# Kernel tuning notes

Hardware: AMD Instinct MI355X
Metric: run time of the kernel (lower is better)

The kernel has to match this reference:

```python
import jax, jax.numpy as jnp
import numpy as np

N = 100000      # nodes
E = 3200000     # directed edges
G = 1024        # graphs in batch


def setup_inputs() -> dict:
    key = jax.random.key(0)
    ks = jax.random.split(key, 12)
    x = jax.random.normal(ks[0], (N, 4), dtype=jnp.float32)
    edge_index = jax.random.randint(ks[1], (2, E), 0, N, dtype=jnp.int64)
    batch = jnp.sort(jax.random.randint(ks[2], (N,), 0, G, dtype=jnp.int64))
    s = 0.1
    return {
        'x': x, 'edge_index': edge_index, 'batch': batch,
        'W_emb': jax.random.normal(ks[3], (4, 1), jnp.float32) * s,
        'b_emb': jax.random.normal(ks[4], (4,), jnp.float32) * s,
        'W1': jax.random.normal(ks[5], (16, 7), jnp.float32) * s,
        'b1': jax.random.normal(ks[6], (16,), jnp.float32) * s,
        'W2': jax.random.normal(ks[7], (8, 16), jnp.float32) * s,
        'b2': jax.random.normal(ks[8], (8,), jnp.float32) * s,
        'W3': jax.random.normal(ks[9], (1, 8), jnp.float32) * s,
        'b3': jax.random.normal(ks[10], (1,), jnp.float32) * s,
    }


def _gcn_norm(edge_index, n):
    # add self-loops (PyG GCNConv default)
    loops = jnp.arange(n, dtype=edge_index.dtype)
    row = jnp.concatenate([edge_index[0], loops])  # source
    col = jnp.concatenate([edge_index[1], loops])  # target
    deg = jax.ops.segment_sum(jnp.ones_like(col, dtype=jnp.float32), col, num_segments=n)
    dinv = jnp.where(deg > 0, deg ** -0.5, 0.0)
    norm = dinv[row] * dinv[col]
    return row, col, norm


def _gcn_conv(h, W, b, row, col, norm, n):
    h = h @ W.T                                   # [n, out]
    msg = h[row] * norm[:, None]                  # gather + scale
    out = jax.ops.segment_sum(msg, col, num_segments=n)
    return out + b


def reference(x, edge_index, batch, W_emb, b_emb, W1, b1, W2, b2, W3, b3):
    row, col, norm = _gcn_norm(edge_index, N)
    atoms_vector = x[:, :1]
    atoms_xyz = x[:, 1:]
    one_hot_emb = atoms_vector @ W_emb.T + b_emb          # [N, 4]
    h = jnp.concatenate([one_hot_emb, atoms_xyz], axis=1) # [N, 7]
    h = jnp.tanh(_gcn_conv(h, W1, b1, row, col, norm, N)) # [N, 16]
    # dropout is identity in eval mode
    h = jnp.tanh(_gcn_conv(h, W2, b2, row, col, norm, N)) # [N, 8]
    # scatter-mean readout over graphs
    sums = jax.ops.segment_sum(h, batch, num_segments=G)
    cnts = jax.ops.segment_sum(jnp.ones((h.shape[0],), h.dtype), batch, num_segments=G)
    pooled = sums / jnp.maximum(cnts, 1.0)[:, None]       # [G, 8]
    return pooled @ W3.T + b3                             # [G, 1]
```

## Files before the change

kernel.cpp:

```cpp
#include <hip/hip_runtime.h>
#include <hip/hip_fp16.h>


constexpr int BLK  = 256;
constexpr int NPB  = 256;
constexpr int NBMX = 512;
constexpr int CAPB = 9216;
constexpr int PBLK = 512;
constexpr int CAPS = 6144;
constexpr int EPT  = 12;
constexpr int SBLK = 512;
constexpr int NIT4 = 5;
constexpr float S8 = 64.0f;

__global__ void k_place(const int4* __restrict__ row4, const int4* __restrict__ col4,
                        int* __restrict__ bucketCnt, unsigned int* __restrict__ data,
                        int E, int NB) {
    __shared__ unsigned int stage[CAPS];
    __shared__ int pos[NBMX], sstart[NBMX], lbase[NBMX];
    __shared__ int wsum[8];
    int t = threadIdx.x;
    int lane = t & 63, w = t >> 6;
    int begin = blockIdx.x * CAPS;
    int end = min(E, begin + CAPS);
    int csize = end - begin;
    int q0 = begin >> 2, q1 = end >> 2;
    if (t < NBMX) pos[t] = 0;
    __syncthreads();
    unsigned int ent[EPT];
    int meta[EPT];
#pragma unroll
    for (int it = 0; it < EPT / 4; it++) {
        int i = q0 + t + it * PBLK;
        bool ok = i < q1;
        int4 c = ok ? col4[i] : make_int4(0, 0, 0, 0);
        int4 r = ok ? row4[i] : make_int4(0, 0, 0, 0);
#pragma unroll
        for (int k = 0; k < 4; k++) {
            int cc = ((const int*)&c)[k];
            int rr = ((const int*)&r)[k];
            int b = cc >> 8;
            int o = ok ? atomicAdd(&pos[b], 1) : 0;
            ent[it * 4 + k] = ((unsigned int)(cc & 255) << 17) | (unsigned int)rr;
            meta[it * 4 + k] = ok ? ((b << 13) | o) : -1;
        }
    }
    __syncthreads();
    int v = pos[t];
    int sc = v;
#pragma unroll
    for (int off = 1; off < 64; off <<= 1) {
        int o = __shfl_up(sc, off, 64);
        if (lane >= off) sc += o;
    }
    if (lane == 63) wsum[w] = sc;
    __syncthreads();
    int pre = 0;
#pragma unroll
    for (int i = 0; i < 8; i++) if (i < w) pre += wsum[i];
    int excl = sc + pre - v;
    sstart[t] = excl;
    lbase[t] = v ? atomicAdd(&bucketCnt[t], v) : 0;
    __syncthreads();
#pragma unroll
    for (int k = 0; k < EPT; k++) {
        int m = meta[k];
        if (m >= 0) stage[sstart[m >> 13] + (m & 0x1FFF)] = ent[k];
    }
    __syncthreads();
    for (int k = t; k < csize; k += PBLK) {
        int lo = 0, hi = NB - 1;
        while (lo < hi) { int m = (lo + hi + 1) >> 1; if (sstart[m] <= k) lo = m; else hi = m - 1; }
        data[(unsigned int)lo * CAPB + (unsigned int)(lbase[lo] + (k - sstart[lo]))] = stage[k];
    }
}

__global__ void k_sort_node1(unsigned int* __restrict__ data,
                             const int* __restrict__ bucketCnt,
                             const float4* __restrict__ x,
                             const float* __restrict__ Wemb, const float* __restrict__ bemb,
                             const float* __restrict__ W1,
                             int* __restrict__ rs, int* __restrict__ re,
                             float* __restrict__ dinv, uint4* __restrict__ u1q, int n) {
    __shared__ int pos[NPB], startl[NPB];
    __shared__ int wsum[4];
    int b = blockIdx.x;
    int t = threadIdx.x;
    int base = b * CAPB;
    int cnt = min(bucketCnt[b], CAPB);
    if (t < NPB) pos[t] = 0;
    __syncthreads();
    const uint4* data4 = (const uint4*)(data + base);
    unsigned int ent[NIT4 * 4];
    int off[NIT4 * 4];
#pragma unroll
    for (int it = 0; it < NIT4; it++) {
        int i4 = t + it * SBLK;
        int i = i4 * 4;
        uint4 p4 = (i < cnt) ? data4[i4] : make_uint4(0, 0, 0, 0);
#pragma unroll
        for (int k = 0; k < 4; k++) {
            int idx = it * 4 + k;
            if (i + k < cnt) {
                unsigned int p = ((const unsigned int*)&p4)[k];
                int dloc = (int)(p >> 17);
                int o = atomicAdd(&pos[dloc], 1);
                ent[idx] = p & 0x1FFFF;
                off[idx] = (dloc << 14) | o;
            } else off[idx] = -1;
        }
    }
    __syncthreads();
    int node = b * NPB + t;
    float d = 0.0f;
    if (t < NPB) {
        int lane = t & 63, w = t >> 6;
        int v = pos[t];
        int sc = v;
#pragma unroll
        for (int o = 1; o < 64; o <<= 1) {
            int s = __shfl_up(sc, o, 64);
            if (lane >= o) sc += s;
        }
        if (lane == 63) wsum[w] = sc;
        __syncthreads();
        int pre = 0;
#pragma unroll
        for (int i = 0; i < 4; i++) if (i < w) pre += wsum[i];
        int excl = sc + pre - v;
        startl[t] = excl;
        if (node < n) {
            rs[node] = base + excl;
            re[node] = base + excl + v;
            d = rsqrtf((float)v + 1.0f);
            dinv[node] = d;
        }
    } else {
        __syncthreads();
    }
    __syncthreads();
#pragma unroll
    for (int it = 0; it < NIT4 * 4; it++) {
        int m = off[it];
        if (m >= 0) data[base + startl[m >> 14] + (m & 0x3FFF)] = ent[it];
    }
    if (t < NPB && node < n) {
        float4 xi = x[node];
        float h0[7];
#pragma unroll
        for (int j = 0; j < 4; j++) h0[j] = xi.x * Wemb[j] + bemb[j];
        h0[4] = xi.y; h0[5] = xi.z; h0[6] = xi.w;
        float s[16];
#pragma unroll
        for (int f = 0; f < 16; f++) {
            float tt = 0.0f;
#pragma unroll
            for (int j = 0; j < 7; j++) tt += h0[j] * W1[f * 7 + j];
            s[f] = tt * d * S8;
        }
        unsigned int w0, w1, w2, w3;
        w0 = __builtin_amdgcn_cvt_pk_fp8_f32(s[0],  s[1],  0,  false);
        w0 = __builtin_amdgcn_cvt_pk_fp8_f32(s[2],  s[3],  w0, true);
        w1 = __builtin_amdgcn_cvt_pk_fp8_f32(s[4],  s[5],  0,  false);
        w1 = __builtin_amdgcn_cvt_pk_fp8_f32(s[6],  s[7],  w1, true);
        w2 = __builtin_amdgcn_cvt_pk_fp8_f32(s[8],  s[9],  0,  false);
        w2 = __builtin_amdgcn_cvt_pk_fp8_f32(s[10], s[11], w2, true);
        w3 = __builtin_amdgcn_cvt_pk_fp8_f32(s[12], s[13], 0,  false);
        w3 = __builtin_amdgcn_cvt_pk_fp8_f32(s[14], s[15], w3, true);
        u1q[node] = make_uint4(w0, w1, w2, w3);
    }
}

typedef float vfloat2 __attribute__((vector_size(8)));

__device__ __forceinline__ void dec16_add(uint4 q, float* acc) {
#pragma unroll
    for (int w = 0; w < 4; w++) {
        unsigned int u = ((const unsigned int*)&q)[w];
        vfloat2 lo = __builtin_amdgcn_cvt_pk_f32_fp8(u, false);
        vfloat2 hi = __builtin_amdgcn_cvt_pk_f32_fp8(u, true);
        acc[4 * w + 0] += lo[0]; acc[4 * w + 1] += lo[1];
        acc[4 * w + 2] += hi[0]; acc[4 * w + 3] += hi[1];
    }
}

__global__ void k_agg1(const unsigned int* __restrict__ sorted,
                       const int* __restrict__ rs, const int* __restrict__ re,
                       const uint4* __restrict__ u1q, const float* __restrict__ dinv,
                       const float* __restrict__ b1, const float* __restrict__ W2,
                       uint4* __restrict__ u2q, int n) {
    int tt = blockIdx.x * BLK + threadIdx.x;
    int node = tt >> 2;
    int j = tt & 3;
    if (node >= n) return;
    int s = rs[node], e = re[node];
    float acc[16];
#pragma unroll
    for (int k = 0; k < 16; k++) acc[k] = 0.0f;
    int i = s + j;
    for (; i + 4 < e; i += 8) {
        uint4 q0 = u1q[sorted[i]];
        uint4 q1 = u1q[sorted[i + 4]];
        dec16_add(q0, acc);
        dec16_add(q1, acc);
    }
    if (i < e) {
        uint4 q = u1q[sorted[i]];
        dec16_add(q, acc);
    }
    if (j == 0) {
        uint4 qs = u1q[node];
        dec16_add(qs, acc);
    }
#pragma unroll
    for (int k = 0; k < 16; k++) {
        acc[k] += __shfl_xor(acc[k], 1, 64);
        acc[k] += __shfl_xor(acc[k], 2, 64);
    }
    float d = dinv[node];
    float dS = d * (1.0f / S8);
    float h1[16];
#pragma unroll
    for (int k = 0; k < 16; k++) h1[k] = tanhf(dS * acc[k] + b1[k]);
    float r[8];
#pragma unroll
    for (int g = 0; g < 8; g++) {
        float ttv = 0.0f;
#pragma unroll
        for (int k = 0; k < 16; k++) ttv += h1[k] * W2[g * 16 + k];
        r[g] = ttv * d;
    }
    if (j == 0) {
        union { __half2 h2[4]; uint4 u4; } pk;
#pragma unroll
        for (int q = 0; q < 4; q++) pk.h2[q] = __floats2half2_rn(r[2 * q], r[2 * q + 1]);
        u2q[node] = pk.u4;
    }
}

__global__ void k_agg2_pool(const unsigned int* __restrict__ sorted,
                            const int* __restrict__ rs, const int* __restrict__ re,
                            const uint4* __restrict__ u2q, const float* __restrict__ dinv,
                            const float* __restrict__ b2, const int* __restrict__ batch,
                            float* __restrict__ pooled, float* __restrict__ cnt, int n) {
    int tt = blockIdx.x * BLK + threadIdx.x;
    int node = tt >> 2;
    int j = tt & 3;
    int lane = threadIdx.x & 63;
    bool valid = node < n;
    float h[8];
#pragma unroll
    for (int k = 0; k < 8; k++) h[k] = 0.0f;
    int g = -1;
    float c = 0.0f;
    if (valid) {
        int s = rs[node], e = re[node];
        float acc[8];
#pragma unroll
        for (int k = 0; k < 8; k++) acc[k] = 0.0f;
        int i = s + j;
        for (; i + 4 < e; i += 8) {
            uint4 q0 = u2q[sorted[i]];
            uint4 q1 = u2q[sorted[i + 4]];
            const __half2* p0 = (const __half2*)&q0;
            const __half2* p1 = (const __half2*)&q1;
#pragma unroll
            for (int k = 0; k < 4; k++) {
                float2 a0 = __half22float2(p0[k]);
                float2 a1 = __half22float2(p1[k]);
                acc[2*k]   += a0.x + a1.x;
                acc[2*k+1] += a0.y + a1.y;
            }
        }
        if (i < e) {
            uint4 q = u2q[sorted[i]];
            const __half2* p = (const __half2*)&q;
#pragma unroll
            for (int k = 0; k < 4; k++) {
                float2 a = __half22float2(p[k]);
                acc[2*k]   += a.x;
                acc[2*k+1] += a.y;
            }
        }
        if (j == 0) {
            uint4 qs = u2q[node];
            const __half2* ps = (const __half2*)&qs;
#pragma unroll
            for (int k = 0; k < 4; k++) {
                float2 a = __half22float2(ps[k]);
                acc[2*k]   += a.x;
                acc[2*k+1] += a.y;
            }
        }
#pragma unroll
        for (int k = 0; k < 8; k++) {
            acc[k] += __shfl_xor(acc[k], 1, 64);
            acc[k] += __shfl_xor(acc[k], 2, 64);
        }
        if (j == 0) {
            float d = dinv[node];
#pragma unroll
            for (int k = 0; k < 8; k++) h[k] = tanhf(d * acc[k] + b2[k]);
            g = batch[node];
            c = 1.0f;
        }
    }
#pragma unroll
    for (int off = 4; off < 64; off <<= 1) {
        int gn = __shfl_down(g, off, 64);
        float cn = __shfl_down(c, off, 64);
        float hn[8];
#pragma unroll
        for (int k = 0; k < 8; k++) hn[k] = __shfl_down(h[k], off, 64);
        bool take = (lane + off < 64) && (gn == g);
        if (take) {
            c += cn;
#pragma unroll
            for (int k = 0; k < 8; k++) h[k] += hn[k];
        }
    }
    int gprev = __shfl_up(g, 4, 64);
    bool head = valid && (j == 0) && (lane == 0 || gprev != g);
    if (head) {
#pragma unroll
        for (int k = 0; k < 8; k++) atomicAdd(&pooled[g * 8 + k], h[k]);
        atomicAdd(&cnt[g], c);
    }
}

__global__ void k_out(const float* __restrict__ pooled, const float* __restrict__ cnt,
                      const float* __restrict__ W3, const float* __restrict__ b3,
                      float* __restrict__ out, int G) {
    int g = blockIdx.x * BLK + threadIdx.x;
    if (g >= G) return;
    float c = fmaxf(cnt[g], 1.0f);
    float t = 0.0f;
#pragma unroll
    for (int k = 0; k < 8; k++) t += pooled[g * 8 + k] * W3[k];
    out[g] = t / c + b3[0];
}

extern "C" void kernel_launch(void* const* d_in, const int* in_sizes, int n_in,
                              void* d_out, int out_size, void* d_ws, size_t ws_size,
                              hipStream_t stream) {
    const float* x    = (const float*)d_in[0];
    const int*   ei   = (const int*)d_in[1];
    const int*   batch= (const int*)d_in[2];
    const float* Wemb = (const float*)d_in[3];
    const float* bemb = (const float*)d_in[4];
    const float* W1   = (const float*)d_in[5];
    const float* b1   = (const float*)d_in[6];
    const float* W2   = (const float*)d_in[7];
    const float* b2   = (const float*)d_in[8];
    const float* W3   = (const float*)d_in[9];
    const float* b3   = (const float*)d_in[10];
    float* out = (float*)d_out;

    const int n = in_sizes[2];
    const int E = in_sizes[1] / 2;
    const int G = out_size;
    const int* row = ei;
    const int* col = ei + E;
    const int NB = (n + NPB - 1) / NPB;

    float* ws    = (float*)d_ws;
    float* dinv  = ws;
    uint4* u1q   = (uint4*)(ws + n);
    __half* u2h  = (__half*)(ws + 9 * n);
    int* rs      = (int*)(ws + 13 * n);
    int* re      = rs + n;
    int* bucketCnt = re + n;
    float* pooled  = (float*)(bucketCnt + NBMX);
    float* cnt     = pooled + 8 * G;
    unsigned int* data = (unsigned int*)(cnt + G);

    int gridP = (E + CAPS - 1) / CAPS;
    int gridA = (4 * n + BLK - 1) / BLK;

    hipMemsetAsync(bucketCnt, 0, (NBMX + 8 * G + G) * sizeof(int), stream);
    k_place<<<gridP, PBLK, 0, stream>>>((const int4*)row, (const int4*)col,
                                        bucketCnt, data, E, NB);
    k_sort_node1<<<NB, SBLK, 0, stream>>>(data, bucketCnt, (const float4*)x,
                                          Wemb, bemb, W1, rs, re, dinv, u1q, n);
    k_agg1<<<gridA, BLK, 0, stream>>>(data, rs, re, u1q,
                                      dinv, b1, W2, (uint4*)u2h, n);
    k_agg2_pool<<<gridA, BLK, 0, stream>>>(data, rs, re,
                                           (const uint4*)u2h, dinv, b2,
                                           batch, pooled, cnt, n);
    k_out<<<(G + BLK - 1) / BLK, BLK, 0, stream>>>(pooled, cnt, W3, b3, out, G);
}
```

Baseline: 189.5 us.

## Replicate shared histograms, tag staged entries with bucket, fuse output into pooling kernel

Shared-memory bucket counters in the placement and local-sort kernels are split into four copies indexed by lane group, which reduces LDS atomic contention, and per-copy offsets are rebuilt after the scan. The placement kernel also records each staged entry's bucket id in a shared array, replacing a per-element binary search during the scatter. The final linear layer moves into the pooling kernel through a last-block-done counter, and zeroing of the pooled buffer moves into agg1, which removes a kernel launch and shrinks the memset. This costs extra shared memory and fence/atomic overhead at the end of every block.

Result: slower. 203.9 us (+7.6%).

```diff
diff --git a/kernel.cpp b/kernel.cpp
--- a/kernel.cpp
+++ b/kernel.cpp
@@ -17,15 +17,19 @@
                         int* __restrict__ bucketCnt, unsigned int* __restrict__ data,
                         int E, int NB) {
     __shared__ unsigned int stage[CAPS];
-    __shared__ int pos[NBMX], sstart[NBMX], lbase[NBMX];
+    __shared__ unsigned short stageB[CAPS];
+    __shared__ int pos[4][NBMX];
+    __shared__ int sstart[NBMX], lbase[NBMX];
     __shared__ int wsum[8];
     int t = threadIdx.x;
     int lane = t & 63, w = t >> 6;
+    int rep = (lane >> 4) & 3;
     int begin = blockIdx.x * CAPS;
     int end = min(E, begin + CAPS);
     int csize = end - begin;
     int q0 = begin >> 2, q1 = end >> 2;
-    if (t < NBMX) pos[t] = 0;
+#pragma unroll
+    for (int rr = 0; rr < 4; rr++) pos[rr][t] = 0;
     __syncthreads();
     unsigned int ent[EPT];
     int meta[EPT];
@@ -40,13 +44,14 @@
             int cc = ((const int*)&c)[k];
             int rr = ((const int*)&r)[k];
             int b = cc >> 8;
-            int o = ok ? atomicAdd(&pos[b], 1) : 0;
+            int o = ok ? atomicAdd(&pos[rep][b], 1) : 0;
             ent[it * 4 + k] = ((unsigned int)(cc & 255) << 17) | (unsigned int)rr;
-            meta[it * 4 + k] = ok ? ((b << 13) | o) : -1;
-        }
-    }
-    __syncthreads();
-    int v = pos[t];
+            meta[it * 4 + k] = ok ? ((rep << 22) | (b << 13) | o) : -1;
+        }
+    }
+    __syncthreads();
+    int p0 = pos[0][t], p1 = pos[1][t], p2 = pos[2][t], p3 = pos[3][t];
+    int v = p0 + p1 + p2 + p3;
     int sc = v;
 #pragma unroll
     for (int off = 1; off < 64; off <<= 1) {
@@ -61,17 +66,27 @@
     int excl = sc + pre - v;
     sstart[t] = excl;
     lbase[t] = v ? atomicAdd(&bucketCnt[t], v) : 0;
+    pos[0][t] = 0;
+    pos[1][t] = p0;
+    pos[2][t] = p0 + p1;
+    pos[3][t] = p0 + p1 + p2;
     __syncthreads();
 #pragma unroll
     for (int k = 0; k < EPT; k++) {
         int m = meta[k];
-        if (m >= 0) stage[sstart[m >> 13] + (m & 0x1FFF)] = ent[k];
+        if (m >= 0) {
+            int rr = m >> 22;
+            int b  = (m >> 13) & 0x1FF;
+            int o  = m & 0x1FFF;
+            int idx = sstart[b] + pos[rr][b] + o;
+            stage[idx]  = ent[k];
+            stageB[idx] = (unsigned short)b;
+        }
     }
     __syncthreads();
     for (int k = t; k < csize; k += PBLK) {
-        int lo = 0, hi = NB - 1;
-        while (lo < hi) { int m = (lo + hi + 1) >> 1; if (sstart[m] <= k) lo = m; else hi = m - 1; }
-        data[(unsigned int)lo * CAPB + (unsigned int)(lbase[lo] + (k - sstart[lo]))] = stage[k];
+        int b = stageB[k];
+        data[(unsigned int)b * CAPB + (unsigned int)(lbase[b] + (k - sstart[b]))] = stage[k];
     }
 }
 
@@ -82,13 +97,16 @@
                              const float* __restrict__ W1,
                              int* __restrict__ rs, int* __restrict__ re,
                              float* __restrict__ dinv, uint4* __restrict__ u1q, int n) {
-    __shared__ int pos[NPB], startl[NPB];
+    __shared__ int pos[4][NPB], startl[NPB];
     __shared__ int wsum[4];
     int b = blockIdx.x;
     int t = threadIdx.x;
+    int lane = t & 63;
+    int rep = (lane >> 4) & 3;
     int base = b * CAPB;
     int cnt = min(bucketCnt[b], CAPB);
-    if (t < NPB) pos[t] = 0;
+    ((int*)pos)[t] = 0;
+    ((int*)pos)[t + SBLK] = 0;
     __syncthreads();
     const uint4* data4 = (const uint4*)(data + base);
     unsigned int ent[NIT4 * 4];
@@ -104,9 +122,9 @@
             if (i + k < cnt) {
                 unsigned int p = ((const unsigned int*)&p4)[k];
                 int dloc = (int)(p >> 17);
-                int o = atomicAdd(&pos[dloc], 1);
+                int o = atomicAdd(&pos[rep][dloc], 1);
                 ent[idx] = p & 0x1FFFF;
-                off[idx] = (dloc << 14) | o;
+                off[idx] = (rep << 22) | (dloc << 14) | o;
             } else off[idx] = -1;
         }
     }
@@ -114,8 +132,9 @@
     int node = b * NPB + t;
     float d = 0.0f;
     if (t < NPB) {
-        int lane = t & 63, w = t >> 6;
-        int v = pos[t];
+        int w = t >> 6;
+        int p0 = pos[0][t], p1 = pos[1][t], p2 = pos[2][t], p3 = pos[3][t];
+        int v = p0 + p1 + p2 + p3;
         int sc = v;
 #pragma unroll
         for (int o = 1; o < 64; o <<= 1) {
@@ -129,6 +148,10 @@
         for (int i = 0; i < 4; i++) if (i < w) pre += wsum[i];
         int excl = sc + pre - v;
         startl[t] = excl;
+        pos[0][t] = 0;
+        pos[1][t] = p0;
+        pos[2][t] = p0 + p1;
+        pos[3][t] = p0 + p1 + p2;
         if (node < n) {
             rs[node] = base + excl;
             re[node] = base + excl + v;
@@ -142,7 +165,12 @@
 #pragma unroll
     for (int it = 0; it < NIT4 * 4; it++) {
         int m = off[it];
-        if (m >= 0) data[base + startl[m >> 14] + (m & 0x3FFF)] = ent[it];
+        if (m >= 0) {
+            int rr = (m >> 22) & 3;
+            int dl = (m >> 14) & 255;
+            int o  = m & 0x3FFF;
+            data[base + startl[dl] + pos[rr][dl] + o] = ent[it];
+        }
     }
     if (t < NPB && node < n) {
         float4 xi = x[node];
@@ -188,8 +216,10 @@
                        const int* __restrict__ rs, const int* __restrict__ re,
                        const uint4* __restrict__ u1q, const float* __restrict__ dinv,
                        const float* __restrict__ b1, const float* __restrict__ W2,
-                       uint4* __restrict__ u2q, int n) {
+                       uint4* __restrict__ u2q, float* __restrict__ pooledz,
+                       int n, int G) {
     int tt = blockIdx.x * BLK + threadIdx.x;
+    if (tt < 9 * G) pooledz[tt] = 0.0f;
     int node = tt >> 2;
     int j = tt & 3;
     if (node >= n) return;
@@ -242,7 +272,10 @@
                             const int* __restrict__ rs, const int* __restrict__ re,
                             const uint4* __restrict__ u2q, const float* __restrict__ dinv,
                             const float* __restrict__ b2, const int* __restrict__ batch,
-                            float* __restrict__ pooled, float* __restrict__ cnt, int n) {
+                            float* __restrict__ pooled, float* __restrict__ cnt,
+                            const float* __restrict__ W3, const float* __restrict__ b3,
+                            float* __restrict__ out, unsigned int* __restrict__ doneCnt,
+                            int n, int G) {
     int tt = blockIdx.x * BLK + threadIdx.x;
     int node = tt >> 2;
     int j = tt & 3;
@@ -326,18 +359,24 @@
         for (int k = 0; k < 8; k++) atomicAdd(&pooled[g * 8 + k], h[k]);
         atomicAdd(&cnt[g], c);
     }
-}
-
-__global__ void k_out(const float* __restrict__ pooled, const float* __restrict__ cnt,
-                      const float* __restrict__ W3, const float* __restrict__ b3,
-                      float* __restrict__ out, int G) {
-    int g = blockIdx.x * BLK + threadIdx.x;
-    if (g >= G) return;
-    float c = fmaxf(cnt[g], 1.0f);
-    float t = 0.0f;
-#pragma unroll
-    for (int k = 0; k < 8; k++) t += pooled[g * 8 + k] * W3[k];
-    out[g] = t / c + b3[0];
+    __shared__ int islast;
+    __syncthreads();
+    if (threadIdx.x == 0) {
+        __threadfence();
+        unsigned int v = atomicAdd(doneCnt, 1u);
+        islast = (v == gridDim.x - 1) ? 1 : 0;
+    }
+    __syncthreads();
+    if (islast) {
+        __threadfence();
+        for (int gg = (int)threadIdx.x; gg < G; gg += BLK) {
+            float cc = fmaxf(cnt[gg], 1.0f);
+            float tsum = 0.0f;
+#pragma unroll
+            for (int k = 0; k < 8; k++) tsum += pooled[gg * 8 + k] * W3[k];
+            out[gg] = tsum / cc + b3[0];
+        }
+    }
 }
 
 extern "C" void kernel_launch(void* const* d_in, const int* in_sizes, int n_in,
@@ -370,22 +409,23 @@
     int* rs      = (int*)(ws + 13 * n);
     int* re      = rs + n;
     int* bucketCnt = re + n;
-    float* pooled  = (float*)(bucketCnt + NBMX);
+    unsigned int* doneCnt = (unsigned int*)(bucketCnt + NBMX);
+    float* pooled  = (float*)(bucketCnt + NBMX + 64);
     float* cnt     = pooled + 8 * G;
     unsigned int* data = (unsigned int*)(cnt + G);
 
     int gridP = (E + CAPS - 1) / CAPS;
     int gridA = (4 * n + BLK - 1) / BLK;
 
-    hipMemsetAsync(bucketCnt, 0, (NBMX + 8 * G + G) * sizeof(int), stream);
+    hipMemsetAsync(bucketCnt, 0, (NBMX + 64) * sizeof(int), stream);
     k_place<<<gridP, PBLK, 0, stream>>>((const int4*)row, (const int4*)col,
                                         bucketCnt, data, E, NB);
     k_sort_node1<<<NB, SBLK, 0, stream>>>(data, bucketCnt, (const float4*)x,
                                           Wemb, bemb, W1, rs, re, dinv, u1q, n);
     k_agg1<<<gridA, BLK, 0, stream>>>(data, rs, re, u1q,
-                                      dinv, b1, W2, (uint4*)u2h, n);
+                                      dinv, b1, W2, (uint4*)u2h, pooled, n, G);
     k_agg2_pool<<<gridA, BLK, 0, stream>>>(data, rs, re,
                                            (const uint4*)u2h, dinv, b2,
-                                           batch, pooled, cnt, n);
-    k_out<<<(G + BLK - 1) / BLK, BLK, 0, stream>>>(pooled, cnt, W3, b3, out, G);
-}
+                                           batch, pooled, cnt, W3, b3, out,
+                                           doneCnt, n, G);
+}
```
